# Performance work log

Hardware: AMD Instinct MI355X
Metric: run time of the kernel (lower is better)

Reference implementation:

```python
import jax, jax.numpy as jnp
import numpy as np

N, A, C = 2048, 256, 100   # batch, feat_dim, num_classes
LAT = A // 2               # latent_dim = feat_dim // 2
BN_EPS = 1e-5


def setup_inputs() -> dict:
    key = jax.random.key(0)
    ks = jax.random.split(key, 8)
    s = jax.random.normal(ks[0], (N, A), dtype=jnp.float32)
    y = jax.random.randint(ks[1], (N,), 0, C)
    ratio = jnp.float32(0.5)
    W1 = jax.random.normal(ks[2], (LAT, A), dtype=jnp.float32) / np.sqrt(A)
    b1 = jnp.zeros((LAT,), jnp.float32)
    gamma = jnp.ones((LAT,), jnp.float32)
    beta = jnp.zeros((LAT,), jnp.float32)
    W2 = jax.random.normal(ks[3], (A, LAT), dtype=jnp.float32) / np.sqrt(LAT)
    b2 = jnp.zeros((A,), jnp.float32)
    Wfc = jax.random.normal(ks[4], (C, A), dtype=jnp.float32) / np.sqrt(A)
    bfc = jnp.zeros((C,), jnp.float32)
    # per-class covariance table [C, A, A], symmetric PSD like a real EstimatorCV state
    M = jax.random.normal(ks[5], (C, A, A), dtype=jnp.float32)
    cov = jnp.einsum('cab,cdb->cad', M, M) / A
    return {"s": s, "y": y, "ratio": ratio, "W1": W1, "b1": b1,
            "gamma": gamma, "beta": beta, "W2": W2, "b2": b2,
            "Wfc": Wfc, "bfc": bfc, "cov": cov}


def reference(s, y, ratio, W1, b1, gamma, beta, W2, b2, Wfc, bfc, cov):
    # pred: Linear -> BatchNorm1d (train-mode batch stats) -> ReLU -> Linear -> ReLU
    h = s @ W1.T + b1                                   # [N, LAT]
    mu = jnp.mean(h, axis=0)
    var = jnp.var(h, axis=0)                            # biased, as torch BN
    h = (h - mu) / jnp.sqrt(var + BN_EPS) * gamma + beta
    h = jax.nn.relu(h)
    f = jax.nn.relu(h @ W2.T + b2)                      # [N, A]
    z = f @ Wfc.T + bfc                                 # [N, C]

    # correct_z: diag of (W_i - W_y) cov[y] (W_i - W_y)^T, computed without the
    # wasted off-diagonal bmm of the original
    cov_sg = jax.lax.stop_gradient(cov)                 # cov is detached in source
    Wy = Wfc[y]                                         # [N, A]
    diff = Wfc[None, :, :] - Wy[:, None, :]             # [N, C, A]
    CVy = cov_sg[y]                                     # [N, A, A]
    tmp = jnp.einsum('nca,nab->ncb', diff, CVy)         # [N, C, A]
    sigma2 = jnp.sum(tmp * diff, axis=-1)               # [N, C] = diag of quad form
    return z + ratio * 0.5 * sigma2
```

## Files before the change

### kernel.cpp

```cpp
#include <hip/hip_runtime.h>
#include <hip/hip_bf16.h>

#define Nn  2048
#define Aa  256
#define Cc  100
#define LAT 128
#define BN_EPS 1e-5f

#define OFF_HB   0
#define OFF_SUMS (OFF_HB + Nn*LAT/2)
#define OFF_SP   (OFF_SUMS + 128*256)
#define OFF_W2B  (OFF_SP + 2*Cc*Cc)
#define OFF_WFB  (OFF_W2B + Aa*LAT/2)

typedef __attribute__((ext_vector_type(8))) short bf16x8;
typedef __attribute__((ext_vector_type(4))) float f32x4;

__device__ __forceinline__ short f2bf(float f) {
    return (short)__bfloat16_as_ushort(__float2bfloat16(f));
}
__device__ __forceinline__ float bf2f(short h) {
    return __uint_as_float(((unsigned)(unsigned short)h) << 16);
}

#define DPITCH 264
#define FPITCH 264
#define NWG_A  530

#define KS_DBYTES   (64 * DPITCH * 2)
#define KS_CBYTES   (32 * DPITCH * 2)
#define KS_SMEM     (KS_DBYTES + KS_CBYTES + 4 * 64 * 4)

template<int MSZ>
__device__ __forceinline__ void ks_body2(
    const float* __restrict__ Wfc, const float* __restrict__ cov,
    float* __restrict__ Spart, short* Dlds, short* covT, float (*red)[64],
    int k, int ch, int bh, int t, int w, int il, int q)
{
    const float* covk = cov + (size_t)k * (Aa * Aa);
    const int c0 = ch * 64;
    const int lane = t & 63;

    {
        const int c4 = t & 63;
        float4 wk = *(const float4*)&Wfc[(size_t)k * Aa + c4 * 4];
#pragma unroll
        for (int j = 0; j < MSZ * 4; j++) {
            int row = (t >> 6) + j * 4;
            int g = c0 + row;
            short4 o = {0, 0, 0, 0};
            if (g < Cc) {
                float4 v = *(const float4*)&Wfc[(size_t)g * Aa + c4 * 4];
                o.x = f2bf(v.x - wk.x); o.y = f2bf(v.y - wk.y);
                o.z = f2bf(v.z - wk.z); o.w = f2bf(v.w - wk.w);
            }
            *(short4*)&Dlds[row * DPITCH + c4 * 4] = o;
        }
    }

    float4 pre[8];
#pragma unroll
    for (int i = 0; i < 8; i++)
        pre[i] = *(const float4*)&covk[(size_t)(bh * 128 + w * 8 + i) * Aa + lane * 4];

    __syncthreads();
#pragma unroll
    for (int i = 0; i < 8; i++) {
        short4 o = {f2bf(pre[i].x), f2bf(pre[i].y), f2bf(pre[i].z), f2bf(pre[i].w)};
        *(short4*)&covT[(w * 8 + i) * DPITCH + lane * 4] = o;
    }
    __syncthreads();

    float sacc[MSZ][4];
#pragma unroll
    for (int m = 0; m < MSZ; m++)
#pragma unroll
        for (int r = 0; r < 4; r++) sacc[m][r] = 0.f;

    for (int p = 0; p < 4; p++) {
        if (p < 3) {
#pragma unroll
            for (int i = 0; i < 8; i++)
                pre[i] = *(const float4*)&covk[(size_t)(bh * 128 + (p + 1) * 32 + w * 8 + i) * Aa + lane * 4];
        }

        f32x4 acc[MSZ][2];
#pragma unroll
        for (int m = 0; m < MSZ; m++) {
            acc[m][0] = (f32x4){0.f,0.f,0.f,0.f};
            acc[m][1] = (f32x4){0.f,0.f,0.f,0.f};
        }
#pragma unroll
        for (int sg = 0; sg < 2; sg++) {
            const int a0 = w * 64 + sg * 32 + q * 8;
            bf16x8 bm0 = *(bf16x8*)&covT[il * DPITCH + a0];
            bf16x8 bm1 = *(bf16x8*)&covT[(16 + il) * DPITCH + a0];
#pragma unroll
            for (int m = 0; m < MSZ; m++) {
                bf16x8 am = *(bf16x8*)&Dlds[(m * 16 + il) * DPITCH + a0];
                acc[m][0] = __builtin_amdgcn_mfma_f32_16x16x32_bf16(am, bm0, acc[m][0], 0, 0, 0);
                acc[m][1] = __builtin_amdgcn_mfma_f32_16x16x32_bf16(am, bm1, acc[m][1], 0, 0, 0);
            }
        }
#pragma unroll
        for (int m = 0; m < MSZ; m++)
#pragma unroll
            for (int nf = 0; nf < 2; nf++) {
                const int bcol = bh * 128 + p * 32 + nf * 16 + il;
#pragma unroll
                for (int r = 0; r < 4; r++) {
                    float dv = bf2f(Dlds[(m * 16 + q * 4 + r) * DPITCH + bcol]);
                    sacc[m][r] = fmaf(dv, acc[m][nf][r], sacc[m][r]);
                }
            }
        __syncthreads();
        if (p < 3) {
#pragma unroll
            for (int i = 0; i < 8; i++) {
                short4 o = {f2bf(pre[i].x), f2bf(pre[i].y), f2bf(pre[i].z), f2bf(pre[i].w)};
                *(short4*)&covT[(w * 8 + i) * DPITCH + lane * 4] = o;
            }
            __syncthreads();
        }
    }

#pragma unroll
    for (int m = 0; m < MSZ; m++) {
#pragma unroll
        for (int r = 0; r < 4; r++) {
            float v = sacc[m][r];
            v += __shfl_xor(v, 1);
            v += __shfl_xor(v, 2);
            v += __shfl_xor(v, 4);
            v += __shfl_xor(v, 8);
            if (il == 0) red[w][m * 16 + q * 4 + r] = v;
        }
    }
    __syncthreads();
    if (t < MSZ * 16) {
        int c = c0 + t;
        if (c < Cc)
            Spart[bh * (Cc * Cc) + k * Cc + c] =
                red[0][t] + red[1][t] + red[2][t] + red[3][t];
    }
}

__global__ __launch_bounds__(256) void kA(
    const float* __restrict__ s, const float* __restrict__ W1,
    const float* __restrict__ b1, const float* __restrict__ Wfc,
    const float* __restrict__ W2, const float* __restrict__ cov,
    short* __restrict__ hB, float* __restrict__ sums, float* __restrict__ Spart,
    short* __restrict__ W2b, short* __restrict__ Wfcb)
{
    __shared__ __align__(16) char smem[KS_SMEM];
    const int orig = blockIdx.x;
    const int xcd  = orig % 8;
    const int bid  = (xcd < 2 ? xcd * 67 : 2 * 67 + (xcd - 2) * 66) + orig / 8;
    const int t = threadIdx.x;
    const int w = t >> 6, l = t & 63, il = l & 15, q = l >> 4;

    if (bid < 400) {
        short* Dlds = (short*)smem;
        short* covT = (short*)(smem + KS_DBYTES);
        float (*red)[64] = (float(*)[64])(smem + KS_DBYTES + KS_CBYTES);
        const int k  = bid >> 2;
        const int ch = (bid >> 1) & 1;
        const int bh = bid & 1;
        if (ch == 0)
            ks_body2<4>(Wfc, cov, Spart, Dlds, covT, red, k, 0, bh, t, w, il, q);
        else
            ks_body2<3>(Wfc, cov, Spart, Dlds, covT, red, k, 1, bh, t, w, il, q);
    } else if (bid < 528) {
        const int bid2 = bid - 400;
        const int row0 = bid2 * 16;
        const int colw = w * 32;

        f32x4 acc[2];
        acc[0] = (f32x4){0.f,0.f,0.f,0.f};
        acc[1] = (f32x4){0.f,0.f,0.f,0.f};

        const float* arow = s  + (size_t)(row0 + il) * Aa;
        const float* bp0  = W1 + (size_t)(colw + il) * Aa;
        const float* bp1  = W1 + (size_t)(colw + 16 + il) * Aa;

        float4 pu0 = *(const float4*)&arow[q * 8];
        float4 pu1 = *(const float4*)&arow[q * 8 + 4];
        float4 pv0 = *(const float4*)&bp0[q * 8];
        float4 pv1 = *(const float4*)&bp0[q * 8 + 4];
        float4 px0 = *(const float4*)&bp1[q * 8];
        float4 px1 = *(const float4*)&bp1[q * 8 + 4];

#pragma unroll
        for (int ks = 0; ks < 8; ks++) {
            const float4 u0 = pu0, u1 = pu1, v0 = pv0, v1 = pv1, x0 = px0, x1 = px1;
            if (ks < 7) {
                const int k1n = (ks + 1) * 32 + q * 8;
                pu0 = *(const float4*)&arow[k1n];
                pu1 = *(const float4*)&arow[k1n + 4];
                pv0 = *(const float4*)&bp0[k1n];
                pv1 = *(const float4*)&bp0[k1n + 4];
                px0 = *(const float4*)&bp1[k1n];
                px1 = *(const float4*)&bp1[k1n + 4];
            }
            bf16x8 am;
            am[0]=f2bf(u0.x); am[1]=f2bf(u0.y); am[2]=f2bf(u0.z); am[3]=f2bf(u0.w);
            am[4]=f2bf(u1.x); am[5]=f2bf(u1.y); am[6]=f2bf(u1.z); am[7]=f2bf(u1.w);
            bf16x8 bm0;
            bm0[0]=f2bf(v0.x); bm0[1]=f2bf(v0.y); bm0[2]=f2bf(v0.z); bm0[3]=f2bf(v0.w);
            bm0[4]=f2bf(v1.x); bm0[5]=f2bf(v1.y); bm0[6]=f2bf(v1.z); bm0[7]=f2bf(v1.w);
            bf16x8 bm1;
            bm1[0]=f2bf(x0.x); bm1[1]=f2bf(x0.y); bm1[2]=f2bf(x0.z); bm1[3]=f2bf(x0.w);
            bm1[4]=f2bf(x1.x); bm1[5]=f2bf(x1.y); bm1[6]=f2bf(x1.z); bm1[7]=f2bf(x1.w);
            acc[0] = __builtin_amdgcn_mfma_f32_16x16x32_bf16(am, bm0, acc[0], 0, 0, 0);
            acc[1] = __builtin_amdgcn_mfma_f32_16x16x32_bf16(am, bm1, acc[1], 0, 0, 0);
        }

#pragma unroll
        for (int n = 0; n < 2; n++) {
            const int col = colw + n * 16 + il;
            const float bias = b1[col];
            float s1 = 0.f, s2 = 0.f;
#pragma unroll
            for (int r = 0; r < 4; r++) {
                float v = acc[n][r] + bias;
                hB[(size_t)(row0 + q * 4 + r) * LAT + col] = f2bf(v);
                s1 += v; s2 += v * v;
            }
            s1 += __shfl_xor(s1, 16); s1 += __shfl_xor(s1, 32);
            s2 += __shfl_xor(s2, 16); s2 += __shfl_xor(s2, 32);
            if (q == 0) {
                sums[bid2 * 256 + col]       = s1;
                sums[bid2 * 256 + 128 + col] = s2;
            }
        }
    } else if (bid == 528) {
        for (int i = t * 4; i < Aa * LAT; i += 1024) {
            float4 v = *(const float4*)&W2[i];
            short4 o = {f2bf(v.x), f2bf(v.y), f2bf(v.z), f2bf(v.w)};
            *(short4*)&W2b[i] = o;
        }
    } else {
        for (int i = t * 4; i < 128 * Aa; i += 1024) {
            int row = i >> 8;
            short4 o = {0, 0, 0, 0};
            if (row < Cc) {
                float4 v = *(const float4*)&Wfc[i];
                o.x = f2bf(v.x); o.y = f2bf(v.y); o.z = f2bf(v.z); o.w = f2bf(v.w);
            }
            *(short4*)&Wfcb[i] = o;
        }
    }
}

__global__ __launch_bounds__(256) void kB(
    const short* __restrict__ hB, const float* __restrict__ sums,
    const float* __restrict__ gamma, const float* __restrict__ beta,
    const short* __restrict__ W2b, const float* __restrict__ b2,
    const short* __restrict__ Wfcb, const float* __restrict__ bfc,
    const float* __restrict__ Spart, const int* __restrict__ y,
    const float* __restrict__ ratio, float* __restrict__ out)
{
    __shared__ float scL[LAT], shL[LAT];
    __shared__ float redA[512];
    __shared__ short fLDS[16 * FPITCH];
    const int t = threadIdx.x;
    const int w = t >> 6, l = t & 63, il = l & 15, q = l >> 4;
    const int row0 = blockIdx.x * 16;

    {
        const int chn = t & 127, hf = t >> 7;
        float a1 = 0.f, a2 = 0.f;
#pragma unroll 16
        for (int b = hf * 64; b < hf * 64 + 64; b++) {
            a1 += sums[b * 256 + chn];
            a2 += sums[b * 256 + 128 + chn];
        }
        redA[hf * 256 + chn]       = a1;
        redA[hf * 256 + 128 + chn] = a2;
    }
    __syncthreads();
    if (t < 128) {
        float A1 = redA[t] + redA[256 + t];
        float A2 = redA[128 + t] + redA[384 + t];
        float mu  = A1 * (1.0f / Nn);
        float var = A2 * (1.0f / Nn) - mu * mu;
        float inv = rsqrtf(var + BN_EPS);
        float sc  = gamma[t] * inv;
        scL[t] = sc;
        shL[t] = beta[t] - mu * sc;
    }
    __syncthreads();

    f32x4 acc3[4];
#pragma unroll
    for (int n = 0; n < 4; n++) acc3[n] = (f32x4){0.f,0.f,0.f,0.f};

    const short* arow = hB + (size_t)(row0 + il) * LAT;
#pragma unroll
    for (int ks = 0; ks < 4; ks++) {
        const int k0 = ks * 32 + q * 8;
        bf16x8 ha = *(const bf16x8*)&arow[k0];
        bf16x8 am;
#pragma unroll
        for (int j = 0; j < 8; j++) {
            float fv = fmaf(bf2f(ha[j]), scL[k0 + j], shL[k0 + j]);
            am[j] = f2bf(fmaxf(fv, 0.f));
        }
#pragma unroll
        for (int n = 0; n < 4; n++) {
            const int col = w * 64 + n * 16 + il;
            bf16x8 bm = *(const bf16x8*)&W2b[(size_t)col * LAT + k0];
            acc3[n] = __builtin_amdgcn_mfma_f32_16x16x32_bf16(am, bm, acc3[n], 0, 0, 0);
        }
    }
#pragma unroll
    for (int n = 0; n < 4; n++) {
        const int col = w * 64 + n * 16 + il;
        const float bias = b2[col];
#pragma unroll
        for (int r = 0; r < 4; r++) {
            float v = fmaxf(acc3[n][r] + bias, 0.f);
            fLDS[(q * 4 + r) * FPITCH + col] = f2bf(v);
        }
    }
    __syncthreads();

    f32x4 acc4[2];
    acc4[0] = (f32x4){0.f,0.f,0.f,0.f};
    acc4[1] = (f32x4){0.f,0.f,0.f,0.f};
#pragma unroll
    for (int ks = 0; ks < 8; ks++) {
        const int k0 = ks * 32 + q * 8;
        bf16x8 am = *(const bf16x8*)&fLDS[il * FPITCH + k0];
#pragma unroll
        for (int n = 0; n < 2; n++) {
            const int col = w * 32 + n * 16 + il;
            bf16x8 bm = *(const bf16x8*)&Wfcb[(size_t)col * Aa + k0];
            acc4[n] = __builtin_amdgcn_mfma_f32_16x16x32_bf16(am, bm, acc4[n], 0, 0, 0);
        }
    }

    const float coef = 0.5f * ratio[0];
    const int4 yv4 = *(const int4*)&y[row0 + q * 4];
    const int yr[4] = {yv4.x, yv4.y, yv4.z, yv4.w};

#pragma unroll
    for (int n = 0; n < 2; n++) {
        const int col = w * 32 + n * 16 + il;
        if (col < Cc) {
            const float bias = bfc[col];
#pragma unroll
            for (int r = 0; r < 4; r++) {
                const float* sp = &Spart[yr[r] * Cc + col];
                float sv = sp[0] + sp[Cc * Cc];
                out[(size_t)(row0 + q * 4 + r) * Cc + col] =
                    acc4[n][r] + bias + coef * sv;
            }
        }
    }
}

extern "C" void kernel_launch(void* const* d_in, const int* in_sizes, int n_in,
                              void* d_out, int out_size, void* d_ws, size_t ws_size,
                              hipStream_t stream)
{
    const float* s     = (const float*)d_in[0];
    const int*   y     = (const int*)  d_in[1];
    const float* ratio = (const float*)d_in[2];
    const float* W1    = (const float*)d_in[3];
    const float* b1    = (const float*)d_in[4];
    const float* gamma = (const float*)d_in[5];
    const float* beta  = (const float*)d_in[6];
    const float* W2    = (const float*)d_in[7];
    const float* b2    = (const float*)d_in[8];
    const float* Wfc   = (const float*)d_in[9];
    const float* bfc   = (const float*)d_in[10];
    const float* cov   = (const float*)d_in[11];
    float* out = (float*)d_out;
    float* ws  = (float*)d_ws;

    short* hB    = (short*)(ws + OFF_HB);
    float* sums  = ws + OFF_SUMS;
    float* Spart = ws + OFF_SP;
    short* W2b   = (short*)(ws + OFF_W2B);
    short* Wfcb  = (short*)(ws + OFF_WFB);

    hipLaunchKernelGGL(kA, dim3(NWG_A), dim3(256), 0, stream,
                       s, W1, b1, Wfc, W2, cov, hB, sums, Spart, W2b, Wfcb);
    hipLaunchKernelGGL(kB, dim3(128), dim3(256), 0, stream,
                       hB, sums, gamma, beta, W2b, b2, Wfcb, bfc, Spart, y, ratio, out);
}
```

Before: 31.29 us.

## Reschedule into three kernels so covariance work overlaps MLP tail

Moves the first linear layer and weight conversions into a small prologue kernel. The per-class covariance quadratic-form work then runs in the same launch as the BN/second/third GEMMs, and a final elementwise kernel adds the sigma2 correction into the output. The aim is to hide the MLP tail behind the heavy covariance work instead of serialising it after that work. The cost is an extra launch, an extra read-modify-write pass over the output, and a tiny prologue kernel that leaves most of the GPU idle.

```diff
diff --git a/kernel.cpp b/kernel.cpp
--- a/kernel.cpp
+++ b/kernel.cpp
@@ -25,7 +25,6 @@
 
 #define DPITCH 264
 #define FPITCH 264
-#define NWG_A  530
 
 #define KS_DBYTES   (64 * DPITCH * 2)
 #define KS_CBYTES   (32 * DPITCH * 2)
@@ -145,17 +144,109 @@
     }
 }
 
-__global__ __launch_bounds__(256) void kA(
+__global__ __launch_bounds__(256) void kPre(
     const float* __restrict__ s, const float* __restrict__ W1,
     const float* __restrict__ b1, const float* __restrict__ Wfc,
-    const float* __restrict__ W2, const float* __restrict__ cov,
-    short* __restrict__ hB, float* __restrict__ sums, float* __restrict__ Spart,
+    const float* __restrict__ W2,
+    short* __restrict__ hB, float* __restrict__ sums,
     short* __restrict__ W2b, short* __restrict__ Wfcb)
+{
+    const int bid = blockIdx.x;
+    const int t = threadIdx.x;
+    const int w = t >> 6, l = t & 63, il = l & 15, q = l >> 4;
+
+    if (bid < 128) {
+        const int row0 = bid * 16;
+        const int colw = w * 32;
+
+        f32x4 acc[2];
+        acc[0] = (f32x4){0.f,0.f,0.f,0.f};
+        acc[1] = (f32x4){0.f,0.f,0.f,0.f};
+
+        const float* arow = s  + (size_t)(row0 + il) * Aa;
+        const float* bp0  = W1 + (size_t)(colw + il) * Aa;
+        const float* bp1  = W1 + (size_t)(colw + 16 + il) * Aa;
+
+        float4 pu0 = *(const float4*)&arow[q * 8];
+        float4 pu1 = *(const float4*)&arow[q * 8 + 4];
+        float4 pv0 = *(const float4*)&bp0[q * 8];
+        float4 pv1 = *(const float4*)&bp0[q * 8 + 4];
+        float4 px0 = *(const float4*)&bp1[q * 8];
+        float4 px1 = *(const float4*)&bp1[q * 8 + 4];
+
+#pragma unroll
+        for (int ks = 0; ks < 8; ks++) {
+            const float4 u0 = pu0, u1 = pu1, v0 = pv0, v1 = pv1, x0 = px0, x1 = px1;
+            if (ks < 7) {
+                const int k1n = (ks + 1) * 32 + q * 8;
+                pu0 = *(const float4*)&arow[k1n];
+                pu1 = *(const float4*)&arow[k1n + 4];
+                pv0 = *(const float4*)&bp0[k1n];
+                pv1 = *(const float4*)&bp0[k1n + 4];
+                px0 = *(const float4*)&bp1[k1n];
+                px1 = *(const float4*)&bp1[k1n + 4];
+            }
+            bf16x8 am;
+            am[0]=f2bf(u0.x); am[1]=f2bf(u0.y); am[2]=f2bf(u0.z); am[3]=f2bf(u0.w);
+            am[4]=f2bf(u1.x); am[5]=f2bf(u1.y); am[6]=f2bf(u1.z); am[7]=f2bf(u1.w);
+            bf16x8 bm0;
+            bm0[0]=f2bf(v0.x); bm0[1]=f2bf(v0.y); bm0[2]=f2bf(v0.z); bm0[3]=f2bf(v0.w);
+            bm0[4]=f2bf(v1.x); bm0[5]=f2bf(v1.y); bm0[6]=f2bf(v1.z); bm0[7]=f2bf(v1.w);
+            bf16x8 bm1;
+            bm1[0]=f2bf(x0.x); bm1[1]=f2bf(x0.y); bm1[2]=f2bf(x0.z); bm1[3]=f2bf(x0.w);
+            bm1[4]=f2bf(x1.x); bm1[5]=f2bf(x1.y); bm1[6]=f2bf(x1.z); bm1[7]=f2bf(x1.w);
+            acc[0] = __builtin_amdgcn_mfma_f32_16x16x32_bf16(am, bm0, acc[0], 0, 0, 0);
+            acc[1] = __builtin_amdgcn_mfma_f32_16x16x32_bf16(am, bm1, acc[1], 0, 0, 0);
+        }
+
+#pragma unroll
+        for (int n = 0; n < 2; n++) {
+            const int col = colw + n * 16 + il;
+            const float bias = b1[col];
+            float s1 = 0.f, s2 = 0.f;
+#pragma unroll
+            for (int r = 0; r < 4; r++) {
+                float v = acc[n][r] + bias;
+                hB[(size_t)(row0 + q * 4 + r) * LAT + col] = f2bf(v);
+                s1 += v; s2 += v * v;
+            }
+            s1 += __shfl_xor(s1, 16); s1 += __shfl_xor(s1, 32);
+            s2 += __shfl_xor(s2, 16); s2 += __shfl_xor(s2, 32);
+            if (q == 0) {
+                sums[bid * 256 + col]       = s1;
+                sums[bid * 256 + 128 + col] = s2;
+            }
+        }
+    } else if (bid == 128) {
+        for (int i = t * 4; i < Aa * LAT; i += 1024) {
+            float4 v = *(const float4*)&W2[i];
+            short4 o = {f2bf(v.x), f2bf(v.y), f2bf(v.z), f2bf(v.w)};
+            *(short4*)&W2b[i] = o;
+        }
+    } else {
+        for (int i = t * 4; i < 128 * Aa; i += 1024) {
+            int row = i >> 8;
+            short4 o = {0, 0, 0, 0};
+            if (row < Cc) {
+                float4 v = *(const float4*)&Wfc[i];
+                o.x = f2bf(v.x); o.y = f2bf(v.y); o.z = f2bf(v.z); o.w = f2bf(v.w);
+            }
+            *(short4*)&Wfcb[i] = o;
+        }
+    }
+}
+
+__global__ __launch_bounds__(256) void kMain(
+    const float* __restrict__ Wfc, const float* __restrict__ cov,
+    const short* __restrict__ hB, const float* __restrict__ sums,
+    const float* __restrict__ gamma, const float* __restrict__ beta,
+    const short* __restrict__ W2b, const float* __restrict__ b2,
+    const short* __restrict__ Wfcb, const float* __restrict__ bfc,
+    float* __restrict__ Spart, float* __restrict__ out)
 {
     __shared__ __align__(16) char smem[KS_SMEM];
     const int orig = blockIdx.x;
-    const int xcd  = orig % 8;
-    const int bid  = (xcd < 2 ? xcd * 67 : 2 * 67 + (xcd - 2) * 66) + orig / 8;
+    const int bid  = (orig & 7) * 66 + (orig >> 3);
     const int t = threadIdx.x;
     const int w = t >> 6, l = t & 63, il = l & 15, q = l >> 4;
 
@@ -170,193 +261,113 @@
             ks_body2<4>(Wfc, cov, Spart, Dlds, covT, red, k, 0, bh, t, w, il, q);
         else
             ks_body2<3>(Wfc, cov, Spart, Dlds, covT, red, k, 1, bh, t, w, il, q);
-    } else if (bid < 528) {
-        const int bid2 = bid - 400;
-        const int row0 = bid2 * 16;
-        const int colw = w * 32;
-
-        f32x4 acc[2];
-        acc[0] = (f32x4){0.f,0.f,0.f,0.f};
-        acc[1] = (f32x4){0.f,0.f,0.f,0.f};
-
-        const float* arow = s  + (size_t)(row0 + il) * Aa;
-        const float* bp0  = W1 + (size_t)(colw + il) * Aa;
-        const float* bp1  = W1 + (size_t)(colw + 16 + il) * Aa;
-
-        float4 pu0 = *(const float4*)&arow[q * 8];
-        float4 pu1 = *(const float4*)&arow[q * 8 + 4];
-        float4 pv0 = *(const float4*)&bp0[q * 8];
-        float4 pv1 = *(const float4*)&bp0[q * 8 + 4];
-        float4 px0 = *(const float4*)&bp1[q * 8];
-        float4 px1 = *(const float4*)&bp1[q * 8 + 4];
-
+    } else {
+        float* scL  = (float*)smem;
+        float* shL  = scL + 128;
+        float* redA = shL + 128;
+        short* fLDS = (short*)(redA + 512);
+        const int row0 = (bid - 400) * 16;
+
+        {
+            const int chn = t & 127, hf = t >> 7;
+            float a1 = 0.f, a2 = 0.f;
+#pragma unroll 16
+            for (int b = hf * 64; b < hf * 64 + 64; b++) {
+                a1 += sums[b * 256 + chn];
+                a2 += sums[b * 256 + 128 + chn];
+            }
+            redA[hf * 256 + chn]       = a1;
+            redA[hf * 256 + 128 + chn] = a2;
+        }
+        __syncthreads();
+        if (t < 128) {
+            float A1 = redA[t] + redA[256 + t];
+            float A2 = redA[128 + t] + redA[384 + t];
+            float mu  = A1 * (1.0f / Nn);
+            float var = A2 * (1.0f / Nn) - mu * mu;
+            float inv = rsqrtf(var + BN_EPS);
+            float sc  = gamma[t] * inv;
+            scL[t] = sc;
+            shL[t] = beta[t] - mu * sc;
+        }
+        __syncthreads();
+
+        f32x4 acc3[4];
+#pragma unroll
+        for (int n = 0; n < 4; n++) acc3[n] = (f32x4){0.f,0.f,0.f,0.f};
+
+        const short* arow = hB + (size_t)(row0 + il) * LAT;
+#pragma unroll
+        for (int ks = 0; ks < 4; ks++) {
+            const int k0 = ks * 32 + q * 8;
+            bf16x8 ha = *(const bf16x8*)&arow[k0];
+            bf16x8 am;
+#pragma unroll
+            for (int j = 0; j < 8; j++) {
+                float fv = fmaf(bf2f(ha[j]), scL[k0 + j], shL[k0 + j]);
+                am[j] = f2bf(fmaxf(fv, 0.f));
+            }
+#pragma unroll
+            for (int n = 0; n < 4; n++) {
+                const int col = w * 64 + n * 16 + il;
+                bf16x8 bm = *(const bf16x8*)&W2b[(size_t)col * LAT + k0];
+                acc3[n] = __builtin_amdgcn_mfma_f32_16x16x32_bf16(am, bm, acc3[n], 0, 0, 0);
+            }
+        }
+#pragma unroll
+        for (int n = 0; n < 4; n++) {
+            const int col = w * 64 + n * 16 + il;
+            const float bias = b2[col];
+#pragma unroll
+            for (int r = 0; r < 4; r++) {
+                float v = fmaxf(acc3[n][r] + bias, 0.f);
+                fLDS[(q * 4 + r) * FPITCH + col] = f2bf(v);
+            }
+        }
+        __syncthreads();
+
+        f32x4 acc4[2];
+        acc4[0] = (f32x4){0.f,0.f,0.f,0.f};
+        acc4[1] = (f32x4){0.f,0.f,0.f,0.f};
 #pragma unroll
         for (int ks = 0; ks < 8; ks++) {
-            const float4 u0 = pu0, u1 = pu1, v0 = pv0, v1 = pv1, x0 = px0, x1 = px1;
-            if (ks < 7) {
-                const int k1n = (ks + 1) * 32 + q * 8;
-                pu0 = *(const float4*)&arow[k1n];
-                pu1 = *(const float4*)&arow[k1n + 4];
-                pv0 = *(const float4*)&bp0[k1n];
-                pv1 = *(const float4*)&bp0[k1n + 4];
-                px0 = *(const float4*)&bp1[k1n];
-                px1 = *(const float4*)&bp1[k1n + 4];
-            }
-            bf16x8 am;
-            am[0]=f2bf(u0.x); am[1]=f2bf(u0.y); am[2]=f2bf(u0.z); am[3]=f2bf(u0.w);
-            am[4]=f2bf(u1.x); am[5]=f2bf(u1.y); am[6]=f2bf(u1.z); am[7]=f2bf(u1.w);
-            bf16x8 bm0;
-            bm0[0]=f2bf(v0.x); bm0[1]=f2bf(v0.y); bm0[2]=f2bf(v0.z); bm0[3]=f2bf(v0.w);
-            bm0[4]=f2bf(v1.x); bm0[5]=f2bf(v1.y); bm0[6]=f2bf(v1.z); bm0[7]=f2bf(v1.w);
-            bf16x8 bm1;
-            bm1[0]=f2bf(x0.x); bm1[1]=f2bf(x0.y); bm1[2]=f2bf(x0.z); bm1[3]=f2bf(x0.w);
-            bm1[4]=f2bf(x1.x); bm1[5]=f2bf(x1.y); bm1[6]=f2bf(x1.z); bm1[7]=f2bf(x1.w);
-            acc[0] = __builtin_amdgcn_mfma_f32_16x16x32_bf16(am, bm0, acc[0], 0, 0, 0);
-            acc[1] = __builtin_amdgcn_mfma_f32_16x16x32_bf16(am, bm1, acc[1], 0, 0, 0);
+            const int k0 = ks * 32 + q * 8;
+            bf16x8 am = *(const bf16x8*)&fLDS[il * FPITCH + k0];
+#pragma unroll
+            for (int n = 0; n < 2; n++) {
+                const int col = w * 32 + n * 16 + il;
+                bf16x8 bm = *(const bf16x8*)&Wfcb[(size_t)col * Aa + k0];
+                acc4[n] = __builtin_amdgcn_mfma_f32_16x16x32_bf16(am, bm, acc4[n], 0, 0, 0);
+            }
         }
 
 #pragma unroll
         for (int n = 0; n < 2; n++) {
-            const int col = colw + n * 16 + il;
-            const float bias = b1[col];
-            float s1 = 0.f, s2 = 0.f;
-#pragma unroll
-            for (int r = 0; r < 4; r++) {
-                float v = acc[n][r] + bias;
-                hB[(size_t)(row0 + q * 4 + r) * LAT + col] = f2bf(v);
-                s1 += v; s2 += v * v;
-            }
-            s1 += __shfl_xor(s1, 16); s1 += __shfl_xor(s1, 32);
-            s2 += __shfl_xor(s2, 16); s2 += __shfl_xor(s2, 32);
-            if (q == 0) {
-                sums[bid2 * 256 + col]       = s1;
-                sums[bid2 * 256 + 128 + col] = s2;
-            }
-        }
-    } else if (bid == 528) {
-        for (int i = t * 4; i < Aa * LAT; i += 1024) {
-            float4 v = *(const float4*)&W2[i];
-            short4 o = {f2bf(v.x), f2bf(v.y), f2bf(v.z), f2bf(v.w)};
-            *(short4*)&W2b[i] = o;
-        }
-    } else {
-        for (int i = t * 4; i < 128 * Aa; i += 1024) {
-            int row = i >> 8;
-            short4 o = {0, 0, 0, 0};
-            if (row < Cc) {
-                float4 v = *(const float4*)&Wfc[i];
-                o.x = f2bf(v.x); o.y = f2bf(v.y); o.z = f2bf(v.z); o.w = f2bf(v.w);
-            }
-            *(short4*)&Wfcb[i] = o;
-        }
-    }
-}
-
-__global__ __launch_bounds__(256) void kB(
-    const short* __restrict__ hB, const float* __restrict__ sums,
-    const float* __restrict__ gamma, const float* __restrict__ beta,
-    const short* __restrict__ W2b, const float* __restrict__ b2,
-    const short* __restrict__ Wfcb, const float* __restrict__ bfc,
+            const int col = w * 32 + n * 16 + il;
+            if (col < Cc) {
+                const float bias = bfc[col];
+#pragma unroll
+                for (int r = 0; r < 4; r++) {
+                    out[(size_t)(row0 + q * 4 + r) * Cc + col] = acc4[n][r] + bias;
+                }
+            }
+        }
+    }
+}
+
+__global__ __launch_bounds__(256) void kEpi(
     const float* __restrict__ Spart, const int* __restrict__ y,
     const float* __restrict__ ratio, float* __restrict__ out)
 {
-    __shared__ float scL[LAT], shL[LAT];
-    __shared__ float redA[512];
-    __shared__ short fLDS[16 * FPITCH];
-    const int t = threadIdx.x;
-    const int w = t >> 6, l = t & 63, il = l & 15, q = l >> 4;
-    const int row0 = blockIdx.x * 16;
-
-    {
-        const int chn = t & 127, hf = t >> 7;
-        float a1 = 0.f, a2 = 0.f;
-#pragma unroll 16
-        for (int b = hf * 64; b < hf * 64 + 64; b++) {
-            a1 += sums[b * 256 + chn];
-            a2 += sums[b * 256 + 128 + chn];
-        }
-        redA[hf * 256 + chn]       = a1;
-        redA[hf * 256 + 128 + chn] = a2;
-    }
-    __syncthreads();
-    if (t < 128) {
-        float A1 = redA[t] + redA[256 + t];
-        float A2 = redA[128 + t] + redA[384 + t];
-        float mu  = A1 * (1.0f / Nn);
-        float var = A2 * (1.0f / Nn) - mu * mu;
-        float inv = rsqrtf(var + BN_EPS);
-        float sc  = gamma[t] * inv;
-        scL[t] = sc;
-        shL[t] = beta[t] - mu * sc;
-    }
-    __syncthreads();
-
-    f32x4 acc3[4];
-#pragma unroll
-    for (int n = 0; n < 4; n++) acc3[n] = (f32x4){0.f,0.f,0.f,0.f};
-
-    const short* arow = hB + (size_t)(row0 + il) * LAT;
-#pragma unroll
-    for (int ks = 0; ks < 4; ks++) {
-        const int k0 = ks * 32 + q * 8;
-        bf16x8 ha = *(const bf16x8*)&arow[k0];
-        bf16x8 am;
-#pragma unroll
-        for (int j = 0; j < 8; j++) {
-            float fv = fmaf(bf2f(ha[j]), scL[k0 + j], shL[k0 + j]);
-            am[j] = f2bf(fmaxf(fv, 0.f));
-        }
-#pragma unroll
-        for (int n = 0; n < 4; n++) {
-            const int col = w * 64 + n * 16 + il;
-            bf16x8 bm = *(const bf16x8*)&W2b[(size_t)col * LAT + k0];
-            acc3[n] = __builtin_amdgcn_mfma_f32_16x16x32_bf16(am, bm, acc3[n], 0, 0, 0);
-        }
-    }
-#pragma unroll
-    for (int n = 0; n < 4; n++) {
-        const int col = w * 64 + n * 16 + il;
-        const float bias = b2[col];
-#pragma unroll
-        for (int r = 0; r < 4; r++) {
-            float v = fmaxf(acc3[n][r] + bias, 0.f);
-            fLDS[(q * 4 + r) * FPITCH + col] = f2bf(v);
-        }
-    }
-    __syncthreads();
-
-    f32x4 acc4[2];
-    acc4[0] = (f32x4){0.f,0.f,0.f,0.f};
-    acc4[1] = (f32x4){0.f,0.f,0.f,0.f};
-#pragma unroll
-    for (int ks = 0; ks < 8; ks++) {
-        const int k0 = ks * 32 + q * 8;
-        bf16x8 am = *(const bf16x8*)&fLDS[il * FPITCH + k0];
-#pragma unroll
-        for (int n = 0; n < 2; n++) {
-            const int col = w * 32 + n * 16 + il;
-            bf16x8 bm = *(const bf16x8*)&Wfcb[(size_t)col * Aa + k0];
-            acc4[n] = __builtin_amdgcn_mfma_f32_16x16x32_bf16(am, bm, acc4[n], 0, 0, 0);
-        }
-    }
-
     const float coef = 0.5f * ratio[0];
-    const int4 yv4 = *(const int4*)&y[row0 + q * 4];
-    const int yr[4] = {yv4.x, yv4.y, yv4.z, yv4.w};
-
-#pragma unroll
-    for (int n = 0; n < 2; n++) {
-        const int col = w * 32 + n * 16 + il;
-        if (col < Cc) {
-            const float bias = bfc[col];
-#pragma unroll
-            for (int r = 0; r < 4; r++) {
-                const float* sp = &Spart[yr[r] * Cc + col];
-                float sv = sp[0] + sp[Cc * Cc];
-                out[(size_t)(row0 + q * 4 + r) * Cc + col] =
-                    acc4[n][r] + bias + coef * sv;
-            }
-        }
+    const int i0 = (blockIdx.x * 256 + threadIdx.x) * 4;
+#pragma unroll
+    for (int j = 0; j < 4; j++) {
+        const int i = i0 + j;
+        const int n = i / 100;
+        const int c = i - n * 100;
+        const float sv = Spart[y[n] * Cc + c] + Spart[Cc * Cc + y[n] * Cc + c];
+        out[i] = out[i] + coef * sv;
     }
 }
 
@@ -385,8 +396,11 @@
     short* W2b   = (short*)(ws + OFF_W2B);
     short* Wfcb  = (short*)(ws + OFF_WFB);
 
-    hipLaunchKernelGGL(kA, dim3(NWG_A), dim3(256), 0, stream,
-                       s, W1, b1, Wfc, W2, cov, hB, sums, Spart, W2b, Wfcb);
-    hipLaunchKernelGGL(kB, dim3(128), dim3(256), 0, stream,
-                       hB, sums, gamma, beta, W2b, b2, Wfcb, bfc, Spart, y, ratio, out);
-}
+    hipLaunchKernelGGL(kPre,  dim3(130), dim3(256), 0, stream,
+                       s, W1, b1, Wfc, W2, hB, sums, W2b, Wfcb);
+    hipLaunchKernelGGL(kMain, dim3(528), dim3(256), 0, stream,
+                       Wfc, cov, hB, sums, gamma, beta, W2b, b2, Wfcb, bfc,
+                       Spart, out);
+    hipLaunchKernelGGL(kEpi,  dim3(200), dim3(256), 0, stream,
+                       Spart, y, ratio, out);
+}
```

After: 36.48 us. 16.6% more time.

## Merge class-chunk workgroups so each cov half is read once

Applied to the files above, without the earlier changes.

Each workgroup now handles all 100 class rows (7 MFMA row tiles) for a given class k and half of the covariance, instead of splitting the rows across two workgroups. This removes the duplicate global reads and bf16 conversion of the same covariance slice, roughly halving cov traffic. In exchange there are half as many covariance workgroups, which may underfill the GPU, and register and LDS use per workgroup rises.

```diff
diff --git a/kernel.cpp b/kernel.cpp
--- a/kernel.cpp
+++ b/kernel.cpp
@@ -25,32 +25,29 @@
 
 #define DPITCH 264
 #define FPITCH 264
-#define NWG_A  530
-
-#define KS_DBYTES   (64 * DPITCH * 2)
+#define NWG_A  330
+
+#define KS_DBYTES   (112 * DPITCH * 2)
 #define KS_CBYTES   (32 * DPITCH * 2)
-#define KS_SMEM     (KS_DBYTES + KS_CBYTES + 4 * 64 * 4)
-
-template<int MSZ>
-__device__ __forceinline__ void ks_body2(
+#define KS_SMEM     (KS_DBYTES + KS_CBYTES + 4 * 112 * 4)
+
+__device__ __forceinline__ void ks_body3(
     const float* __restrict__ Wfc, const float* __restrict__ cov,
-    float* __restrict__ Spart, short* Dlds, short* covT, float (*red)[64],
-    int k, int ch, int bh, int t, int w, int il, int q)
+    float* __restrict__ Spart, short* Dlds, short* covT, float (*red)[112],
+    int k, int bh, int t, int w, int il, int q)
 {
     const float* covk = cov + (size_t)k * (Aa * Aa);
-    const int c0 = ch * 64;
     const int lane = t & 63;
 
     {
         const int c4 = t & 63;
         float4 wk = *(const float4*)&Wfc[(size_t)k * Aa + c4 * 4];
 #pragma unroll
-        for (int j = 0; j < MSZ * 4; j++) {
+        for (int j = 0; j < 28; j++) {
             int row = (t >> 6) + j * 4;
-            int g = c0 + row;
             short4 o = {0, 0, 0, 0};
-            if (g < Cc) {
-                float4 v = *(const float4*)&Wfc[(size_t)g * Aa + c4 * 4];
+            if (row < Cc) {
+                float4 v = *(const float4*)&Wfc[(size_t)row * Aa + c4 * 4];
                 o.x = f2bf(v.x - wk.x); o.y = f2bf(v.y - wk.y);
                 o.z = f2bf(v.z - wk.z); o.w = f2bf(v.w - wk.w);
             }
@@ -71,9 +68,9 @@
     }
     __syncthreads();
 
-    float sacc[MSZ][4];
-#pragma unroll
-    for (int m = 0; m < MSZ; m++)
+    float sacc[7][4];
+#pragma unroll
+    for (int m = 0; m < 7; m++)
 #pragma unroll
         for (int r = 0; r < 4; r++) sacc[m][r] = 0.f;
 
@@ -84,9 +81,9 @@
                 pre[i] = *(const float4*)&covk[(size_t)(bh * 128 + (p + 1) * 32 + w * 8 + i) * Aa + lane * 4];
         }
 
-        f32x4 acc[MSZ][2];
-#pragma unroll
-        for (int m = 0; m < MSZ; m++) {
+        f32x4 acc[7][2];
+#pragma unroll
+        for (int m = 0; m < 7; m++) {
             acc[m][0] = (f32x4){0.f,0.f,0.f,0.f};
             acc[m][1] = (f32x4){0.f,0.f,0.f,0.f};
         }
@@ -96,14 +93,14 @@
             bf16x8 bm0 = *(bf16x8*)&covT[il * DPITCH + a0];
             bf16x8 bm1 = *(bf16x8*)&covT[(16 + il) * DPITCH + a0];
 #pragma unroll
-            for (int m = 0; m < MSZ; m++) {
+            for (int m = 0; m < 7; m++) {
                 bf16x8 am = *(bf16x8*)&Dlds[(m * 16 + il) * DPITCH + a0];
                 acc[m][0] = __builtin_amdgcn_mfma_f32_16x16x32_bf16(am, bm0, acc[m][0], 0, 0, 0);
                 acc[m][1] = __builtin_amdgcn_mfma_f32_16x16x32_bf16(am, bm1, acc[m][1], 0, 0, 0);
             }
         }
 #pragma unroll
-        for (int m = 0; m < MSZ; m++)
+        for (int m = 0; m < 7; m++)
 #pragma unroll
             for (int nf = 0; nf < 2; nf++) {
                 const int bcol = bh * 128 + p * 32 + nf * 16 + il;
@@ -125,7 +122,7 @@
     }
 
 #pragma unroll
-    for (int m = 0; m < MSZ; m++) {
+    for (int m = 0; m < 7; m++) {
 #pragma unroll
         for (int r = 0; r < 4; r++) {
             float v = sacc[m][r];
@@ -137,12 +134,9 @@
         }
     }
     __syncthreads();
-    if (t < MSZ * 16) {
-        int c = c0 + t;
-        if (c < Cc)
-            Spart[bh * (Cc * Cc) + k * Cc + c] =
-                red[0][t] + red[1][t] + red[2][t] + red[3][t];
-    }
+    if (t < 112 && t < Cc)
+        Spart[bh * (Cc * Cc) + k * Cc + t] =
+            red[0][t] + red[1][t] + red[2][t] + red[3][t];
 }
 
 __global__ __launch_bounds__(256) void kA(
@@ -155,23 +149,17 @@
     __shared__ __align__(16) char smem[KS_SMEM];
     const int orig = blockIdx.x;
     const int xcd  = orig % 8;
-    const int bid  = (xcd < 2 ? xcd * 67 : 2 * 67 + (xcd - 2) * 66) + orig / 8;
+    const int bid  = (xcd < 2 ? xcd * 42 : 2 * 42 + (xcd - 2) * 41) + orig / 8;
     const int t = threadIdx.x;
     const int w = t >> 6, l = t & 63, il = l & 15, q = l >> 4;
 
-    if (bid < 400) {
+    if (bid < 200) {
         short* Dlds = (short*)smem;
         short* covT = (short*)(smem + KS_DBYTES);
-        float (*red)[64] = (float(*)[64])(smem + KS_DBYTES + KS_CBYTES);
-        const int k  = bid >> 2;
-        const int ch = (bid >> 1) & 1;
-        const int bh = bid & 1;
-        if (ch == 0)
-            ks_body2<4>(Wfc, cov, Spart, Dlds, covT, red, k, 0, bh, t, w, il, q);
-        else
-            ks_body2<3>(Wfc, cov, Spart, Dlds, covT, red, k, 1, bh, t, w, il, q);
-    } else if (bid < 528) {
-        const int bid2 = bid - 400;
+        float (*red)[112] = (float(*)[112])(smem + KS_DBYTES + KS_CBYTES);
+        ks_body3(Wfc, cov, Spart, Dlds, covT, red, bid >> 1, bid & 1, t, w, il, q);
+    } else if (bid < 328) {
+        const int bid2 = bid - 200;
         const int row0 = bid2 * 16;
         const int colw = w * 32;
 
@@ -233,7 +221,7 @@
                 sums[bid2 * 256 + 128 + col] = s2;
             }
         }
-    } else if (bid == 528) {
+    } else if (bid == 328) {
         for (int i = t * 4; i < Aa * LAT; i += 1024) {
             float4 v = *(const float4*)&W2[i];
             short4 o = {f2bf(v.x), f2bf(v.y), f2bf(v.z), f2bf(v.w)};
```

After: 37.80 us. 20.8% more time.
